# Kernel tuning notes

Measured on AMD Instinct MI355X. Metric: run time of the kernel, lower is better.

## Reference

```python
import jax, jax.numpy as jnp
import numpy as np

DIM = 1024

def setup_inputs() -> dict:
    key = jax.random.key(0)
    k1, k2, k3, k4 = jax.random.split(key, 4)
    B, L, D = 32, 2048, DIM
    x = jax.random.normal(k1, (B, D), dtype=jnp.float32)
    context = jax.random.normal(k2, (B, L, D), dtype=jnp.float32)
    # linear_concatWa: Linear(2*dim, dim, bias=False) -> weight [dim, 2*dim]
    Wa = jax.random.normal(k3, (D, 2 * D), dtype=jnp.float32) * (1.0 / np.sqrt(2 * D))
    # linear_concatVa: Linear(dim, 1, bias=False) -> weight [1, dim]
    Va = jax.random.normal(k4, (1, D), dtype=jnp.float32) * (1.0 / np.sqrt(D))
    return {"x": x, "context": context, "Wa": Wa, "Va": Va}


def reference(x, context, Wa, Va):
    # concat-mode additive (Bahdanau) attention.
    # Wa @ cat(ht, hs) == ht @ Wa[:, :D].T + hs @ Wa[:, D:].T  (avoids materializing concat)
    D = x.shape[-1]
    Wa_t, Wa_s = Wa[:, :D], Wa[:, D:]              # each [D, D]
    ht_proj = jnp.einsum('bd,kd->bk', x, Wa_t)     # [B, D]
    hs_proj = jnp.einsum('bld,kd->blk', context, Wa_s)  # [B, L, D]
    hidden = jnp.tanh(ht_proj[:, None, :] + hs_proj)    # [B, L, D]
    scores = jnp.einsum('blk,ok->bl', hidden, Va)       # [B, L]  (Va: [1, D])
    attn = jax.nn.softmax(scores, axis=-1)               # [B, L]
    weighted = jnp.einsum('bl,bld->bd', attn, context)   # [B, D]
    return weighted, attn
```

## Files before the change

kernel.cpp:

```cpp
#include <hip/hip_runtime.h>
#include <hip/hip_bf16.h>
#include <cstdint>
#include <cstddef>

#define DIM 1024
#define B_SZ 32
#define L_SZ 2048

#define BM 128
#define BN 128

#define CVT_BLOCKS 8192
#define HT_BLOCKS  512
#define WA_BLOCKS  512

typedef __attribute__((ext_vector_type(8))) short bf16x8;
typedef __attribute__((ext_vector_type(4))) float floatx4;

static __device__ __forceinline__ unsigned cvt2_bf16_rne(float a, float b) {
    unsigned ua = __builtin_bit_cast(unsigned, a);
    unsigned ub = __builtin_bit_cast(unsigned, b);
    ua = (ua + 0x7FFFu + ((ua >> 16) & 1u)) >> 16;
    ub = (ub + 0x7FFFu + ((ub >> 16) & 1u)) >> 16;
    return ua | (ub << 16);
}

static __device__ __forceinline__ float bf2f(unsigned u16) {
    return __builtin_bit_cast(float, u16 << 16);
}

static __device__ __forceinline__ float tanh_fast(float x) {
    float e = __expf(2.0f * x);
    return 1.0f - 2.0f * __builtin_amdgcn_rcpf(e + 1.0f);
}

static __device__ __forceinline__ void gld_lds16(const void* g, void* lds) {
    __builtin_amdgcn_global_load_lds(
        (const __attribute__((address_space(1))) unsigned int*)g,
        (__attribute__((address_space(3))) unsigned int*)lds,
        16, 0, 0);
}

__global__ __launch_bounds__(256) void pre_kernel(
    const float* __restrict__ x, const float* __restrict__ ctx,
    const float* __restrict__ Wa,
    unsigned short* __restrict__ ctxB, unsigned short* __restrict__ WaB,
    float* __restrict__ ht, float* __restrict__ scores,
    float* __restrict__ weighted)
{
    const int bid = blockIdx.x, t = threadIdx.x;

    if (bid < CVT_BLOCKS) {
        const long n8 = (long)B_SZ * L_SZ * DIM / 8;
        const long stride = (long)CVT_BLOCKS * 256;
        for (long i = (long)bid * 256 + t; i < n8; i += stride) {
            const float4 a = ((const float4*)ctx)[i * 2];
            const float4 b = ((const float4*)ctx)[i * 2 + 1];
            uint4 o;
            o.x = cvt2_bf16_rne(a.x, a.y);
            o.y = cvt2_bf16_rne(a.z, a.w);
            o.z = cvt2_bf16_rne(b.x, b.y);
            o.w = cvt2_bf16_rne(b.z, b.w);
            ((uint4*)ctxB)[i] = o;
        }
    } else if (bid < CVT_BLOCKS + HT_BLOCKS) {
        const int lb = bid - CVT_BLOCKS;
        const int gi = lb * 256 + t;
        if (gi < B_SZ * L_SZ) scores[gi] = 0.f;
        const int b = lb >> 4, kb = lb & 15;
        __shared__ float xs[DIM];
        for (int i = t; i < DIM; i += 256) xs[i] = x[b * DIM + i];
        __syncthreads();
        const int wave = t >> 6, lane = t & 63;
        const float4* xs4 = (const float4*)xs;
        for (int kk = 0; kk < 16; ++kk) {
            const int k = kb * 64 + wave * 16 + kk;
            const float4* wr = (const float4*)(Wa + (size_t)k * (2 * DIM));
            float s = 0.f;
            #pragma unroll
            for (int d = 0; d < DIM / 4; d += 64) {
                const float4 w4 = wr[d + lane];
                const float4 x4 = xs4[d + lane];
                s += w4.x * x4.x + w4.y * x4.y + w4.z * x4.z + w4.w * x4.w;
            }
            #pragma unroll
            for (int off = 32; off > 0; off >>= 1) s += __shfl_xor(s, off);
            if (lane == 0) ht[b * DIM + k] = s;
        }
    } else {
        const int lb = bid - CVT_BLOCKS - HT_BLOCKS;
        const int i = lb * 256 + t;
        if (i < B_SZ * DIM) weighted[i] = 0.f;
        const int k = i >> 7, dc = i & 127;
        const float* s = Wa + (size_t)k * (2 * DIM) + DIM + dc * 8;
        const float4 a = ((const float4*)s)[0];
        const float4 b4 = ((const float4*)s)[1];
        uint4 o;
        o.x = cvt2_bf16_rne(a.x, a.y);
        o.y = cvt2_bf16_rne(a.z, a.w);
        o.z = cvt2_bf16_rne(b4.x, b4.y);
        o.w = cvt2_bf16_rne(b4.z, b4.w);
        ((uint4*)(WaB + (size_t)k * DIM + dc * 8))[0] = o;
    }
}

__global__ __launch_bounds__(256) void gemm_score_bf16(
    const unsigned short* __restrict__ A, const unsigned short* __restrict__ Bm,
    const float* __restrict__ Va, const float* __restrict__ ht,
    float* __restrict__ scores)
{
    __shared__ __align__(16) unsigned short As[BM * 64];
    __shared__ __align__(16) unsigned short Bs[BN * 64];
    const int t = threadIdx.x;
    const int n0 = blockIdx.x * BN;
    const int m0 = blockIdx.y * BM;
    const int lane = t & 63, wave = t >> 6;
    const int l15 = lane & 15, quad = lane >> 4;
    const int wm = (wave >> 1) * 64, wn = (wave & 1) * 64;

    const int lr = lane >> 3;
    const int lc = (lane & 7) ^ lr;
    const size_t aRow = (size_t)(m0 + wave * 32 + lr);
    const size_t bRow = (size_t)(n0 + wave * 32 + lr);

    floatx4 acc[4][4];
    #pragma unroll
    for (int i = 0; i < 4; ++i)
        #pragma unroll
        for (int j = 0; j < 4; ++j) acc[i][j] = (floatx4)0.f;

    for (int k0 = 0; k0 < DIM; k0 += 64) {
        #pragma unroll
        for (int q = 0; q < 4; ++q) {
            gld_lds16(A + (aRow + q * 8) * DIM + k0 + lc * 8,
                      &As[(wave * 32 + q * 8) * 64]);
            gld_lds16(Bm + (bRow + q * 8) * DIM + k0 + lc * 8,
                      &Bs[(wave * 32 + q * 8) * 64]);
        }
        __syncthreads();

        bf16x8 af[2][4], bv[2][4];
        #pragma unroll
        for (int kb = 0; kb < 2; ++kb) {
            #pragma unroll
            for (int i = 0; i < 4; ++i) {
                const int r = wm + i * 16 + l15;
                const int c = (kb * 4 + quad) ^ (r & 7);
                af[kb][i] = *(const bf16x8*)&As[r * 64 + c * 8];
            }
            #pragma unroll
            for (int j = 0; j < 4; ++j) {
                const int r = wn + j * 16 + l15;
                const int c = (kb * 4 + quad) ^ (r & 7);
                bv[kb][j] = *(const bf16x8*)&Bs[r * 64 + c * 8];
            }
        }
        #pragma unroll
        for (int kb = 0; kb < 2; ++kb)
            #pragma unroll
            for (int i = 0; i < 4; ++i)
                #pragma unroll
                for (int j = 0; j < 4; ++j)
                    acc[i][j] = __builtin_amdgcn_mfma_f32_16x16x32_bf16(
                        af[kb][i], bv[kb][j], acc[i][j], 0, 0, 0);
        __syncthreads();
    }

    const int bb = m0 >> 11;
    float htv[4], vav[4];
    #pragma unroll
    for (int j = 0; j < 4; ++j) {
        const int ng = n0 + wn + j * 16 + l15;
        htv[j] = ht[bb * DIM + ng];
        vav[j] = Va[ng];
    }
    #pragma unroll
    for (int i = 0; i < 4; ++i) {
        #pragma unroll
        for (int r = 0; r < 4; ++r) {
            float s = 0.f;
            #pragma unroll
            for (int j = 0; j < 4; ++j)
                s += tanh_fast(acc[i][j][r] + htv[j]) * vav[j];
            s += __shfl_xor(s, 8);
            s += __shfl_xor(s, 4);
            s += __shfl_xor(s, 2);
            s += __shfl_xor(s, 1);
            if (l15 == 0)
                atomicAdd(&scores[m0 + wm + i * 16 + quad * 4 + r], s);
        }
    }
}

__global__ __launch_bounds__(256) void post_kernel(
    const float* __restrict__ scores, const unsigned short* __restrict__ ctxB,
    float* __restrict__ attn, float* __restrict__ weighted)
{
    const int b = blockIdx.x, slice = blockIdx.y, t = threadIdx.x;
    const float* sc = scores + b * L_SZ;
    __shared__ float red[256];
    __shared__ float att[128];

    float m = -1e30f;
    for (int l = t; l < L_SZ; l += 256) m = fmaxf(m, sc[l]);
    red[t] = m; __syncthreads();
    for (int s = 128; s > 0; s >>= 1) { if (t < s) red[t] = fmaxf(red[t], red[t + s]); __syncthreads(); }
    m = red[0]; __syncthreads();
    float sum = 0.f;
    for (int l = t; l < L_SZ; l += 256) sum += __expf(sc[l] - m);
    red[t] = sum; __syncthreads();
    for (int s = 128; s > 0; s >>= 1) { if (t < s) red[t] += red[t + s]; __syncthreads(); }
    const float inv = 1.0f / red[0];

    const int l0 = slice * 128;
    if (t < 128) {
        const float av = __expf(sc[l0 + t] - m) * inv;
        att[t] = av;
        attn[b * L_SZ + l0 + t] = av;
    }
    __syncthreads();

    const unsigned short* cb = ctxB + ((size_t)b * L_SZ + l0) * DIM + t * 4;
    float a0 = 0.f, a1 = 0.f, a2 = 0.f, a3 = 0.f;
    for (int l = 0; l < 128; ++l) {
        const float a = att[l];
        const uint2 v = *(const uint2*)(cb + (size_t)l * DIM);
        a0 += a * bf2f(v.x & 0xFFFFu);
        a1 += a * bf2f(v.x >> 16);
        a2 += a * bf2f(v.y & 0xFFFFu);
        a3 += a * bf2f(v.y >> 16);
    }
    float* o = weighted + b * DIM + t * 4;
    atomicAdd(o + 0, a0);
    atomicAdd(o + 1, a1);
    atomicAdd(o + 2, a2);
    atomicAdd(o + 3, a3);
}

#define LDS_STRIDE 40
__global__ __launch_bounds__(256) void ht_kernel_fb(const float* __restrict__ x,
                                                    const float* __restrict__ Wa,
                                                    float* __restrict__ ht,
                                                    float* __restrict__ scores,
                                                    float* __restrict__ weighted) {
    const int b = blockIdx.x, kb = blockIdx.y, t = threadIdx.x;
    const int gidx = (b * 16 + kb) * 256 + t;
    if (gidx < B_SZ * L_SZ) scores[gidx] = 0.f;
    if (gidx < B_SZ * DIM) weighted[gidx] = 0.f;
    __shared__ float xs[DIM];
    for (int i = t; i < DIM; i += 256) xs[i] = x[b * DIM + i];
    __syncthreads();
    const int wave = t >> 6, lane = t & 63;
    for (int kk = 0; kk < 16; ++kk) {
        const int k = kb * 64 + wave * 16 + kk;
        const float* wr = Wa + (size_t)k * (2 * DIM);
        float s = 0.f;
        #pragma unroll
        for (int d = 0; d < DIM; d += 64) s += xs[d + lane] * wr[d + lane];
        #pragma unroll
        for (int off = 32; off > 0; off >>= 1) s += __shfl_xor(s, off);
        if (lane == 0) ht[b * DIM + k] = s;
    }
}

__global__ __launch_bounds__(256, 2) void gemm_score_kernel(
    const float* __restrict__ ctx, const float* __restrict__ Wa,
    const float* __restrict__ Va, const float* __restrict__ ht,
    float* __restrict__ scores)
{
    __shared__ unsigned short As[BM * LDS_STRIDE];
    __shared__ unsigned short Bs[BN * LDS_STRIDE];
    const int t = threadIdx.x;
    const int n0 = blockIdx.x * BN;
    const int m0 = blockIdx.y * BM;
    const int lane = t & 63, wave = t >> 6;
    const int l15 = lane & 15, quad = lane >> 4;
    const int wm = (wave >> 1) * 64, wn = (wave & 1) * 64;
    const int srow = t >> 3;
    const int scol = (t & 7) * 4;
    const float* aBase = ctx + (size_t)(m0 + srow) * DIM + scol;
    const float* bBase = Wa + (size_t)(n0 + srow) * (2 * DIM) + DIM + scol;

    floatx4 acc[4][4];
    #pragma unroll
    for (int i = 0; i < 4; ++i)
        #pragma unroll
        for (int j = 0; j < 4; ++j) acc[i][j] = (floatx4)0.f;

    for (int k0 = 0; k0 < DIM; k0 += 32) {
        __syncthreads();
        #pragma unroll
        for (int r = 0; r < 4; ++r) {
            const float4 va = *(const float4*)(aBase + (size_t)(r * 32) * DIM + k0);
            const float4 vb = *(const float4*)(bBase + (size_t)(r * 32) * (2 * DIM) + k0);
            *(uint2*)&As[(srow + r * 32) * LDS_STRIDE + scol] =
                make_uint2(cvt2_bf16_rne(va.x, va.y), cvt2_bf16_rne(va.z, va.w));
            *(uint2*)&Bs[(srow + r * 32) * LDS_STRIDE + scol] =
                make_uint2(cvt2_bf16_rne(vb.x, vb.y), cvt2_bf16_rne(vb.z, vb.w));
        }
        __syncthreads();
        bf16x8 af[4], bfr[4];
        #pragma unroll
        for (int i = 0; i < 4; ++i)
            af[i] = *(const bf16x8*)&As[(wm + i * 16 + l15) * LDS_STRIDE + quad * 8];
        #pragma unroll
        for (int j = 0; j < 4; ++j)
            bfr[j] = *(const bf16x8*)&Bs[(wn + j * 16 + l15) * LDS_STRIDE + quad * 8];
        #pragma unroll
        for (int i = 0; i < 4; ++i)
            #pragma unroll
            for (int j = 0; j < 4; ++j)
                acc[i][j] = __builtin_amdgcn_mfma_f32_16x16x32_bf16(af[i], bfr[j], acc[i][j], 0, 0, 0);
    }
    const int bb = m0 >> 11;
    float htv[4], vav[4];
    #pragma unroll
    for (int j = 0; j < 4; ++j) {
        const int ng = n0 + wn + j * 16 + l15;
        htv[j] = ht[bb * DIM + ng];
        vav[j] = Va[ng];
    }
    #pragma unroll
    for (int i = 0; i < 4; ++i) {
        #pragma unroll
        for (int r = 0; r < 4; ++r) {
            float s = 0.f;
            #pragma unroll
            for (int j = 0; j < 4; ++j)
                s += tanh_fast(acc[i][j][r] + htv[j]) * vav[j];
            s += __shfl_xor(s, 8);
            s += __shfl_xor(s, 4);
            s += __shfl_xor(s, 2);
            s += __shfl_xor(s, 1);
            if (l15 == 0)
                atomicAdd(&scores[m0 + wm + i * 16 + quad * 4 + r], s);
        }
    }
}

__global__ __launch_bounds__(256) void post_kernel_fb(
    const float* __restrict__ scores, const float* __restrict__ ctx,
    float* __restrict__ attn, float* __restrict__ weighted)
{
    const int b = blockIdx.x, slice = blockIdx.y, t = threadIdx.x;
    const float* sc = scores + b * L_SZ;
    __shared__ float red[256];
    __shared__ float att[128];
    float m = -1e30f;
    for (int l = t; l < L_SZ; l += 256) m = fmaxf(m, sc[l]);
    red[t] = m; __syncthreads();
    for (int s = 128; s > 0; s >>= 1) { if (t < s) red[t] = fmaxf(red[t], red[t + s]); __syncthreads(); }
    m = red[0]; __syncthreads();
    float sum = 0.f;
    for (int l = t; l < L_SZ; l += 256) sum += __expf(sc[l] - m);
    red[t] = sum; __syncthreads();
    for (int s = 128; s > 0; s >>= 1) { if (t < s) red[t] += red[t + s]; __syncthreads(); }
    const float inv = 1.0f / red[0];
    const int l0 = slice * 128;
    if (t < 128) {
        const float av = __expf(sc[l0 + t] - m) * inv;
        att[t] = av;
        attn[b * L_SZ + l0 + t] = av;
    }
    __syncthreads();
    const float* cb = ctx + ((size_t)b * L_SZ + l0) * DIM + t * 4;
    float4 w = make_float4(0.f, 0.f, 0.f, 0.f);
    for (int l = 0; l < 128; ++l) {
        const float a = att[l];
        const float4 c = *(const float4*)(cb + (size_t)l * DIM);
        w.x += a * c.x; w.y += a * c.y; w.z += a * c.z; w.w += a * c.w;
    }
    float* o = weighted + b * DIM + t * 4;
    atomicAdd(o + 0, w.x);
    atomicAdd(o + 1, w.y);
    atomicAdd(o + 2, w.z);
    atomicAdd(o + 3, w.w);
}

extern "C" void kernel_launch(void* const* d_in, const int* in_sizes, int n_in,
                              void* d_out, int out_size, void* d_ws, size_t ws_size,
                              hipStream_t stream) {
    const float* x   = (const float*)d_in[0];
    const float* ctx = (const float*)d_in[1];
    const float* Wa  = (const float*)d_in[2];
    const float* Va  = (const float*)d_in[3];

    float* out      = (float*)d_out;
    float* weighted = out;
    float* attn     = out + B_SZ * DIM;

    float* scores = (float*)d_ws;
    float* ht     = scores + B_SZ * L_SZ;

    const size_t base = (size_t)(B_SZ * L_SZ + B_SZ * DIM) * sizeof(float);
    const size_t need = base + (size_t)DIM * DIM * 2
                      + (size_t)B_SZ * L_SZ * DIM * 2;

    if (ws_size >= need) {
        unsigned short* WaB  = (unsigned short*)((char*)d_ws + base);
        unsigned short* ctxB = WaB + (size_t)DIM * DIM;
        pre_kernel<<<CVT_BLOCKS + HT_BLOCKS + WA_BLOCKS, 256, 0, stream>>>(
            x, ctx, Wa, ctxB, WaB, ht, scores, weighted);
        gemm_score_bf16<<<dim3(DIM / BN, (B_SZ * L_SZ) / BM), 256, 0, stream>>>(
            ctxB, WaB, Va, ht, scores);
        post_kernel<<<dim3(B_SZ, 16), 256, 0, stream>>>(scores, ctxB, attn, weighted);
    } else {
        ht_kernel_fb<<<dim3(B_SZ, 16), 256, 0, stream>>>(x, Wa, ht, scores, weighted);
        gemm_score_kernel<<<dim3(DIM / BN, (B_SZ * L_SZ) / BM), 256, 0, stream>>>(
            ctx, Wa, Va, ht, scores);
        post_kernel_fb<<<dim3(B_SZ, 16), 256, 0, stream>>>(scores, ctx, attn, weighted);
    }
}
```

Baseline: 601.2 us.

## Replace score GEMM with 256x256 tile, 8-wave, 8-phase pipelined kernel

Replaces the 128x128 single-buffered GEMM with a 256x256 tile kernel using 512 threads. It double-buffers LDS half-tiles, interleaves global-to-LDS loads with MFMA phases using explicit vmcnt waits and barriers, and raises MFMA wave priority. Blocks are remapped so that consecutive blocks are spread across groups of eight, which is meant to improve L2 locality. The goal is to hide global load latency and raise arithmetic intensity, at the cost of 128 KB of LDS per block, more registers, and more barriers.

Result: faster. 586.8 us (-2.4%).

```diff
diff --git a/kernel.cpp b/kernel.cpp
--- a/kernel.cpp
+++ b/kernel.cpp
@@ -40,6 +40,9 @@
         (__attribute__((address_space(3))) unsigned int*)lds,
         16, 0, 0);
 }
+
+#define VMCNT(n) asm volatile("s_waitcnt vmcnt(" #n ")" ::: "memory")
+#define BARRIER() __builtin_amdgcn_s_barrier()
 
 __global__ __launch_bounds__(256) void pre_kernel(
     const float* __restrict__ x, const float* __restrict__ ctx,
@@ -104,92 +107,194 @@
     }
 }
 
-__global__ __launch_bounds__(256) void gemm_score_bf16(
+static __device__ __forceinline__ void frag_loads_a(
+    const unsigned short* sh, int wr, int l15, int quad, bf16x8 (&af)[4][2])
+{
+    #pragma unroll
+    for (int i = 0; i < 4; ++i) {
+        const int r = wr + i * 16 + l15;
+        #pragma unroll
+        for (int kb = 0; kb < 2; ++kb) {
+            const int c = (kb * 4 + quad) ^ (r & 7);
+            af[i][kb] = *(const bf16x8*)&sh[r * 64 + c * 8];
+        }
+    }
+}
+
+static __device__ __forceinline__ void frag_loads_b(
+    const unsigned short* sh, int wc, int l15, int quad, bf16x8 (&bv)[2][2])
+{
+    #pragma unroll
+    for (int j = 0; j < 2; ++j) {
+        const int r = wc + j * 16 + l15;
+        #pragma unroll
+        for (int kb = 0; kb < 2; ++kb) {
+            const int c = (kb * 4 + quad) ^ (r & 7);
+            bv[j][kb] = *(const bf16x8*)&sh[r * 64 + c * 8];
+        }
+    }
+}
+
+static __device__ __forceinline__ void mma16(
+    floatx4 (&acc)[4][2], const bf16x8 (&af)[4][2], const bf16x8 (&bv)[2][2])
+{
+    __builtin_amdgcn_s_setprio(1);
+    #pragma unroll
+    for (int kb = 0; kb < 2; ++kb)
+        #pragma unroll
+        for (int i = 0; i < 4; ++i)
+            #pragma unroll
+            for (int j = 0; j < 2; ++j)
+                acc[i][j] = __builtin_amdgcn_mfma_f32_16x16x32_bf16(
+                    af[i][kb], bv[j][kb], acc[i][j], 0, 0, 0);
+    __builtin_amdgcn_s_setprio(0);
+}
+
+static __device__ __forceinline__ void stage_half(
+    const unsigned short* __restrict__ g, unsigned short* lds, int t, int wave)
+{
+    #pragma unroll
+    for (int q = 0; q < 2; ++q) {
+        const int ch = q * 512 + t;
+        const int lr = ch >> 3;
+        const int lc = (ch & 7) ^ (lr & 7);
+        gld_lds16(g + (size_t)lr * DIM + lc * 8, lds + (q * 512 + wave * 64) * 8);
+    }
+}
+
+__global__ __launch_bounds__(512, 2) void gemm_score_8ph(
     const unsigned short* __restrict__ A, const unsigned short* __restrict__ Bm,
     const float* __restrict__ Va, const float* __restrict__ ht,
     float* __restrict__ scores)
 {
-    __shared__ __align__(16) unsigned short As[BM * 64];
-    __shared__ __align__(16) unsigned short Bs[BN * 64];
+    __shared__ __align__(16) unsigned short As[2][2][128 * 64];
+    __shared__ __align__(16) unsigned short Bs[2][2][128 * 64];
+
+    const int bid = blockIdx.x;
+    const int logical = (bid & 7) * 128 + (bid >> 3);
+    const int m0 = (logical >> 2) * 256;
+    const int n0 = (logical & 3) * 256;
+
     const int t = threadIdx.x;
-    const int n0 = blockIdx.x * BN;
-    const int m0 = blockIdx.y * BM;
     const int lane = t & 63, wave = t >> 6;
     const int l15 = lane & 15, quad = lane >> 4;
-    const int wm = (wave >> 1) * 64, wn = (wave & 1) * 64;
-
-    const int lr = lane >> 3;
-    const int lc = (lane & 7) ^ lr;
-    const size_t aRow = (size_t)(m0 + wave * 32 + lr);
-    const size_t bRow = (size_t)(n0 + wave * 32 + lr);
-
-    floatx4 acc[4][4];
-    #pragma unroll
-    for (int i = 0; i < 4; ++i)
-        #pragma unroll
-        for (int j = 0; j < 4; ++j) acc[i][j] = (floatx4)0.f;
-
-    for (int k0 = 0; k0 < DIM; k0 += 64) {
-        #pragma unroll
-        for (int q = 0; q < 4; ++q) {
-            gld_lds16(A + (aRow + q * 8) * DIM + k0 + lc * 8,
-                      &As[(wave * 32 + q * 8) * 64]);
-            gld_lds16(Bm + (bRow + q * 8) * DIM + k0 + lc * 8,
-                      &Bs[(wave * 32 + q * 8) * 64]);
-        }
-        __syncthreads();
-
-        bf16x8 af[2][4], bv[2][4];
-        #pragma unroll
-        for (int kb = 0; kb < 2; ++kb) {
-            #pragma unroll
-            for (int i = 0; i < 4; ++i) {
-                const int r = wm + i * 16 + l15;
-                const int c = (kb * 4 + quad) ^ (r & 7);
-                af[kb][i] = *(const bf16x8*)&As[r * 64 + c * 8];
+    const int wr = (wave >> 2) * 64;
+    const int wc = (wave & 3) * 32;
+
+    const unsigned short* Ag = A + (size_t)m0 * DIM;
+    const unsigned short* Bg = Bm + (size_t)n0 * DIM;
+
+    floatx4 acc[4][4][2];
+    #pragma unroll
+    for (int q = 0; q < 4; ++q)
+        #pragma unroll
+        for (int i = 0; i < 4; ++i)
+            #pragma unroll
+            for (int j = 0; j < 2; ++j) acc[q][i][j] = (floatx4)0.f;
+
+    bf16x8 af[4][2], bv[2][2];
+
+    stage_half(Ag, &As[0][0][0], t, wave);
+    stage_half(Bg, &Bs[0][0][0], t, wave);
+    stage_half(Bg + (size_t)128 * DIM, &Bs[0][1][0], t, wave);
+    stage_half(Ag + (size_t)128 * DIM, &As[0][1][0], t, wave);
+    stage_half(Ag + 64, &As[1][0][0], t, wave);
+    stage_half(Bg + (size_t)128 * DIM + 64, &Bs[1][1][0], t, wave);
+    VMCNT(4);
+    BARRIER();
+
+    for (int it = 0; it < 8; ++it) {
+        const int k1 = (2 * it + 1) * 64;
+        const int k2 = (2 * it + 2) * 64;
+        const int k3 = (2 * it + 3) * 64;
+        const bool more = (it < 7);
+
+        frag_loads_a(&As[0][0][0], wr, l15, quad, af);
+        frag_loads_b(&Bs[0][0][0], wc, l15, quad, bv);
+        stage_half(Bg + k1, &Bs[1][0][0], t, wave);
+        stage_half(Ag + (size_t)128 * DIM + k1, &As[1][1][0], t, wave);
+        BARRIER();
+        mma16(acc[0], af, bv);
+        BARRIER();
+
+        frag_loads_b(&Bs[0][1][0], wc, l15, quad, bv);
+        BARRIER();
+        mma16(acc[1], af, bv);
+        BARRIER();
+
+        frag_loads_a(&As[0][1][0], wr, l15, quad, af);
+        BARRIER();
+        mma16(acc[3], af, bv);
+        BARRIER();
+
+        frag_loads_b(&Bs[0][0][0], wc, l15, quad, bv);
+        if (more) { stage_half(Ag + k2, &As[0][0][0], t, wave); VMCNT(2); }
+        else      { VMCNT(0); }
+        BARRIER();
+        mma16(acc[2], af, bv);
+        BARRIER();
+
+        frag_loads_a(&As[1][0][0], wr, l15, quad, af);
+        frag_loads_b(&Bs[1][0][0], wc, l15, quad, bv);
+        if (more) stage_half(Bg + (size_t)128 * DIM + k2, &Bs[0][1][0], t, wave);
+        BARRIER();
+        mma16(acc[0], af, bv);
+        BARRIER();
+
+        frag_loads_b(&Bs[1][1][0], wc, l15, quad, bv);
+        if (more) stage_half(Ag + (size_t)128 * DIM + k2, &As[0][1][0], t, wave);
+        BARRIER();
+        mma16(acc[1], af, bv);
+        BARRIER();
+
+        frag_loads_a(&As[1][1][0], wr, l15, quad, af);
+        if (more) {
+            stage_half(Bg + k2, &Bs[0][0][0], t, wave);
+            stage_half(Ag + k3, &As[1][0][0], t, wave);
+        }
+        BARRIER();
+        mma16(acc[3], af, bv);
+        BARRIER();
+
+        frag_loads_b(&Bs[1][0][0], wc, l15, quad, bv);
+        if (more) {
+            stage_half(Bg + (size_t)128 * DIM + k3, &Bs[1][1][0], t, wave);
+            VMCNT(4);
+        }
+        BARRIER();
+        mma16(acc[2], af, bv);
+        BARRIER();
+    }
+
+    const int bb = m0 >> 11;
+    float htv[2][2], vav[2][2];
+    #pragma unroll
+    for (int qc = 0; qc < 2; ++qc)
+        #pragma unroll
+        for (int j = 0; j < 2; ++j) {
+            const int ng = n0 + qc * 128 + wc + j * 16 + l15;
+            htv[qc][j] = ht[bb * DIM + ng];
+            vav[qc][j] = Va[ng];
+        }
+    #pragma unroll
+    for (int qr = 0; qr < 2; ++qr)
+        #pragma unroll
+        for (int i = 0; i < 4; ++i)
+            #pragma unroll
+            for (int r = 0; r < 4; ++r) {
+                float s = 0.f;
+                #pragma unroll
+                for (int qc = 0; qc < 2; ++qc)
+                    #pragma unroll
+                    for (int j = 0; j < 2; ++j)
+                        s += tanh_fast(acc[qr * 2 + qc][i][j][r] + htv[qc][j]) * vav[qc][j];
+                s += __shfl_xor(s, 8);
+                s += __shfl_xor(s, 4);
+                s += __shfl_xor(s, 2);
+                s += __shfl_xor(s, 1);
+                if (l15 == 0)
+                    atomicAdd(&scores[m0 + qr * 128 + wr + i * 16 + quad * 4 + r], s);
             }
-            #pragma unroll
-            for (int j = 0; j < 4; ++j) {
-                const int r = wn + j * 16 + l15;
-                const int c = (kb * 4 + quad) ^ (r & 7);
-                bv[kb][j] = *(const bf16x8*)&Bs[r * 64 + c * 8];
-            }
-        }
-        #pragma unroll
-        for (int kb = 0; kb < 2; ++kb)
-            #pragma unroll
-            for (int i = 0; i < 4; ++i)
-                #pragma unroll
-                for (int j = 0; j < 4; ++j)
-                    acc[i][j] = __builtin_amdgcn_mfma_f32_16x16x32_bf16(
-                        af[kb][i], bv[kb][j], acc[i][j], 0, 0, 0);
-        __syncthreads();
-    }
-
-    const int bb = m0 >> 11;
-    float htv[4], vav[4];
-    #pragma unroll
-    for (int j = 0; j < 4; ++j) {
-        const int ng = n0 + wn + j * 16 + l15;
-        htv[j] = ht[bb * DIM + ng];
-        vav[j] = Va[ng];
-    }
-    #pragma unroll
-    for (int i = 0; i < 4; ++i) {
-        #pragma unroll
-        for (int r = 0; r < 4; ++r) {
-            float s = 0.f;
-            #pragma unroll
-            for (int j = 0; j < 4; ++j)
-                s += tanh_fast(acc[i][j][r] + htv[j]) * vav[j];
-            s += __shfl_xor(s, 8);
-            s += __shfl_xor(s, 4);
-            s += __shfl_xor(s, 2);
-            s += __shfl_xor(s, 1);
-            if (l15 == 0)
-                atomicAdd(&scores[m0 + wm + i * 16 + quad * 4 + r], s);
-        }
-    }
 }
 
 __global__ __launch_bounds__(256) void post_kernel(
@@ -401,7 +506,7 @@
         unsigned short* ctxB = WaB + (size_t)DIM * DIM;
         pre_kernel<<<CVT_BLOCKS + HT_BLOCKS + WA_BLOCKS, 256, 0, stream>>>(
             x, ctx, Wa, ctxB, WaB, ht, scores, weighted);
-        gemm_score_bf16<<<dim3(DIM / BN, (B_SZ * L_SZ) / BM), 256, 0, stream>>>(
+        gemm_score_8ph<<<(B_SZ * L_SZ / 256) * (DIM / 256), 512, 0, stream>>>(
             ctxB, WaB, Va, ht, scores);
         post_kernel<<<dim3(B_SZ, 16), 256, 0, stream>>>(scores, ctxB, attn, weighted);
     } else {
```
